# Kernel optimization log

Measured on AMD Instinct MI355X. Metric: run time of the kernel, lower is better.

## Reference

```python
import jax, jax.numpy as jnp
import numpy as np

HEADS = 8
B, N, DIM = 8, 1024, 128  # n must be a perfect square (H=W=32)
LN_EPS = 1e-5


def _region_means(xg):
    """Four-quadrant region means per position via integral image.
    xg: [b,H,W,d] -> [b,H,W,4,d]. For position (h,w) the torch code pools:
      r1 = x[:, :h+1, :w+1], r2 = x[:, :h+1, w:], r3 = x[:, h:, :w+1], r4 = x[:, h:, w:]
    """
    b, H, W, d = xg.shape
    # padded 2D prefix sum: P[:, i, j] = sum over rows<i, cols<j
    P = jnp.pad(jnp.cumsum(jnp.cumsum(xg, axis=1), axis=2),
                ((0, 0), (1, 0), (1, 0), (0, 0)))
    r1 = P[:, 1:, 1:]                                              # sum x[:h+1,:w+1]
    r2 = P[:, 1:, -1:] - P[:, 1:, :-1]                             # sum x[:h+1, w:]
    r3 = P[:, -1:, 1:] - P[:, :-1, 1:]                             # sum x[h:, :w+1]
    r4 = P[:, -1:, -1:] - P[:, :-1, -1:] - P[:, -1:, :-1] + P[:, :-1, :-1]
    ah = jnp.arange(H, dtype=xg.dtype)
    aw = jnp.arange(W, dtype=xg.dtype)
    hp1 = (ah + 1.0)[:, None]   # h+1
    wp1 = (aw + 1.0)[None, :]   # w+1
    hr = (H - ah)[:, None]      # H-h
    wr = (W - aw)[None, :]      # W-w
    c1 = (hp1 * wp1)[None, :, :, None]
    c2 = (hp1 * wr)[None, :, :, None]
    c3 = (hr * wp1)[None, :, :, None]
    c4 = (hr * wr)[None, :, :, None]
    return jnp.stack([r1 / c1, r2 / c2, r3 / c3, r4 / c4], axis=3)


def setup_inputs() -> dict:
    key = jax.random.key(0)
    ks = jax.random.split(key, 10)
    s = 0.02
    return {
        "x": jax.random.normal(ks[0], (B, N, DIM), jnp.float32),
        "ln_g": jnp.ones((DIM,), jnp.float32),
        "ln_b": jnp.zeros((DIM,), jnp.float32),
        "Wqkv": jax.random.normal(ks[1], (DIM, 3 * HEADS * DIM), jnp.float32) * s,
        "bqkv": jax.random.normal(ks[2], (3 * HEADS * DIM,), jnp.float32) * s,
        "Wq": jax.random.normal(ks[3], (DIM, DIM), jnp.float32) * s,
        "Wk": jax.random.normal(ks[4], (DIM, DIM), jnp.float32) * s,
        "Wv": jax.random.normal(ks[5], (DIM, DIM), jnp.float32) * s,
        "Wo": jax.random.normal(ks[6], (DIM, DIM), jnp.float32) * s,
        "bo": jax.random.normal(ks[7], (DIM,), jnp.float32) * s,
        "Wout": jax.random.normal(ks[8], (HEADS * DIM, DIM), jnp.float32) * s,
        "bout": jax.random.normal(ks[9], (DIM,), jnp.float32) * s,
    }


def reference(x, ln_g, ln_b, Wqkv, bqkv, Wq, Wk, Wv, Wo, bo, Wout, bout):
    b, n, dim = x.shape
    H = W = int(n ** 0.5)
    # LayerNorm
    mu = jnp.mean(x, axis=-1, keepdims=True)
    var = jnp.mean(jnp.square(x - mu), axis=-1, keepdims=True)
    xn = (x - mu) * jax.lax.rsqrt(var + LN_EPS) * ln_g + ln_b
    # qkv projection; only q is actually used downstream (k,v chunks are dead)
    qkv = xn @ Wqkv + bqkv
    q = qkv[..., : HEADS * dim].reshape(b, n, HEADS, dim).transpose(0, 2, 1, 3)  # [b,h,n,d]
    # region features, identical across heads -> keep unbroadcast [b,n,4,d]
    regions = _region_means(xn.reshape(b, H, W, dim)).reshape(b, n, 4, dim)
    # RegionAggregator
    qh = q @ Wq                                   # [b,h,n,d]
    k = jnp.einsum('bnrd,de->bnre', regions, Wk)  # [b,n,4,d]
    v = jnp.einsum('bnrd,de->bnre', regions, Wv)
    scale = (dim // HEADS) ** -0.5
    attn = jax.nn.softmax(jnp.einsum('bhnd,bnrd->bhnr', qh, k) * scale, axis=-1)
    agg = jnp.einsum('bhnr,bnrd->bhnd', attn, v)
    out = agg @ Wo + bo                           # [b,h,n,d]
    out = out.transpose(0, 2, 1, 3).reshape(b, n, HEADS * dim)
    return out @ Wout + bout
```

## Files before the change

kernel.cpp:

```cpp
#include <hip/hip_runtime.h>
#include <hip/hip_bf16.h>
#include <stdint.h>

#define HEADS 8
#define NN 1024
#define DIM 128
#define HW 32
#define LN_EPS 1e-5f

typedef __hip_bfloat16 bf16;
typedef __bf16 bf16x8 __attribute__((ext_vector_type(8)));
typedef float floatx4 __attribute__((ext_vector_type(4)));

__device__ __forceinline__ float b2f(bf16 v){ return __bfloat162float(v); }
__device__ __forceinline__ bf16 f2b(float v){ return __float2bfloat16(v); }

__device__ __forceinline__ float ldin(const void* p, size_t i, int f){
    return f ? ((const float*)p)[i] : b2f(((const bf16*)p)[i]);
}
__device__ __forceinline__ float4 ldin4(const void* p, size_t i, int f){
    if (f) return *reinterpret_cast<const float4*>((const float*)p + i);
    ushort4 u = *reinterpret_cast<const ushort4*>((const bf16*)p + i);
    float4 r;
    r.x = b2f(*(bf16*)&u.x); r.y = b2f(*(bf16*)&u.y);
    r.z = b2f(*(bf16*)&u.z); r.w = b2f(*(bf16*)&u.w);
    return r;
}
__device__ __forceinline__ int dtf(const void* g){
    return (((const uint32_t*)g)[0] == 0x3F800000u) ? 1 : 0;
}

__global__ __launch_bounds__(256) void ln_kernel(const void* __restrict__ x,
                                                 const void* __restrict__ g,
                                                 const void* __restrict__ bta,
                                                 bf16* __restrict__ xn){
    int f = dtf(g);
    int row = blockIdx.x*4 + (threadIdx.x >> 6);
    int lane = threadIdx.x & 63;
    size_t base = (size_t)row*DIM;
    float v0 = ldin(x, base+lane,    f);
    float v1 = ldin(x, base+lane+64, f);
    float s = v0+v1, ss = v0*v0+v1*v1;
    for (int o=32;o;o>>=1){ s += __shfl_xor(s,o,64); ss += __shfl_xor(ss,o,64); }
    float mu = s * (1.0f/DIM);
    float var = ss * (1.0f/DIM) - mu*mu;
    float rs = rsqrtf(var + LN_EPS);
    float y0 = (v0-mu)*rs*ldin(g,lane,f)    + ldin(bta,lane,f);
    float y1 = (v1-mu)*rs*ldin(g,lane+64,f) + ldin(bta,lane+64,f);
    xn[base+lane]    = f2b(y0);
    xn[base+lane+64] = f2b(y1);
}

__global__ __launch_bounds__(128) void rowscan_kernel(const bf16* __restrict__ xn,
                                                      float* __restrict__ P){
    int b = blockIdx.x >> 5, h = blockIdx.x & 31, c = threadIdx.x;
    const bf16* xr = xn + ((size_t)(b*NN + h*HW))*DIM + c;
    float* Pr = P + ((size_t)(b*NN + h*HW))*DIM + c;
    float run = 0.f;
    for (int w=0; w<HW; w++){ run += b2f(xr[(size_t)w*DIM]); Pr[(size_t)w*DIM] = run; }
}

__global__ __launch_bounds__(128) void colscan_kernel(float* __restrict__ P){
    int b = blockIdx.x >> 5, w = blockIdx.x & 31, c = threadIdx.x;
    float* Pc = P + ((size_t)(b*NN + w))*DIM + c;
    float run = 0.f;
    for (int h=0; h<HW; h++){
        size_t o = (size_t)h*HW*DIM;
        run += Pc[o]; Pc[o] = run;
    }
}

__global__ __launch_bounds__(256) void prep_kernel(const void* __restrict__ Wqkv,
                                                   const void* __restrict__ bqkv,
                                                   const void* __restrict__ Wq,
                                                   const void* __restrict__ Wk,
                                                   const void* __restrict__ Wv,
                                                   const void* __restrict__ Wo,
                                                   const void* __restrict__ bo,
                                                   const void* __restrict__ Wout,
                                                   const void* __restrict__ ln_g,
                                                   bf16* __restrict__ WhT,
                                                   bf16* __restrict__ WhoT,
                                                   bf16* __restrict__ WkvT,
                                                   float* __restrict__ bq,
                                                   float* __restrict__ bfin_part){
    __shared__ float S1[128][132];
    __shared__ float S2[8][132];
    int f = dtf(ln_g);
    int t = threadIdx.x;
    int blk = blockIdx.x;
    if (blk < 128){
        int h = blk >> 4, dc = blk & 15;
#pragma unroll
        for (int i=0;i<16;i++){
            int idx4 = (t + i*256)*4;
            int k = idx4 >> 7, e = idx4 & 127;
            *reinterpret_cast<float4*>(&S1[k][e]) = ldin4(Wq, idx4, f);
        }
        {
            int idx4 = t*4;
            int dl = idx4 >> 7, k = idx4 & 127;
            *reinterpret_cast<float4*>(&S2[dl][k]) =
                ldin4(Wqkv, (size_t)(dc*8+dl)*3072 + h*128 + k, f);
        }
        __syncthreads();
        int d = t & 7;
        int e0 = (t >> 3) * 4;
        float acc[4] = {0.f,0.f,0.f,0.f};
        for (int k=0;k<128;k++){
            float a = S2[d][k];
            float4 wv = *reinterpret_cast<const float4*>(&S1[k][e0]);
            acc[0] += a*wv.x; acc[1] += a*wv.y; acc[2] += a*wv.z; acc[3] += a*wv.w;
        }
#pragma unroll
        for (int i=0;i<4;i++)
            WhT[(size_t)(h*128 + e0 + i)*128 + dc*8 + d] = f2b(acc[i]);
    } else if (blk < 256){
        int h = (blk-128) >> 4, dc = (blk-128) & 15;
#pragma unroll
        for (int i=0;i<16;i++){
            int idx4 = (t + i*256)*4;
            int k = idx4 >> 7, e = idx4 & 127;
            *reinterpret_cast<float4*>(&S1[k][e]) =
                ldin4(Wout, (size_t)(h*128 + k)*128 + e, f);
        }
        {
            int idx4 = t*4;
            int dl = idx4 >> 7, k = idx4 & 127;
            *reinterpret_cast<float4*>(&S2[dl][k]) =
                ldin4(Wo, (size_t)(dc*8+dl)*128 + k, f);
        }
        __syncthreads();
        int d = t & 7;
        int e0 = (t >> 3) * 4;
        float acc[4] = {0.f,0.f,0.f,0.f};
        for (int k=0;k<128;k++){
            float a = S2[d][k];
            float4 wv = *reinterpret_cast<const float4*>(&S1[k][e0]);
            acc[0] += a*wv.x; acc[1] += a*wv.y; acc[2] += a*wv.z; acc[3] += a*wv.w;
        }
#pragma unroll
        for (int i=0;i<4;i++)
            WhoT[(size_t)(e0 + i)*1024 + h*128 + dc*8 + d] = f2b(acc[i]);
    } else {
        int sub = blk - 256;
        if (sub < 8){
            int h = sub;
            int e = t & 127, kh = t >> 7;
            float s = 0.f;
            for (int k=kh*64; k<kh*64+64; k++)
                s += ldin(bqkv, h*128 + k, f) * ldin(Wq, (size_t)k*128 + e, f);
            S1[kh][e] = s;
            __syncthreads();
            if (t < 128) bq[h*128 + t] = S1[0][t] + S1[1][t];
        } else if (sub < 16){
            int h = sub - 8;
            if (t < 128) S2[0][t] = ldin(bo, t, f);
            __syncthreads();
            int e = t & 127, half = t >> 7;
            float s = 0.f;
            for (int k = half*64; k < half*64 + 64; k++)
                s += S2[0][k] * ldin(Wout, (size_t)(h*128 + k)*128 + e, f);
            S1[half][e] = s;
            __syncthreads();
            if (t < 128) bfin_part[h*128 + t] = S1[0][t] + S1[1][t];
        } else {
            const void* W = (sub == 16) ? Wk : Wv;
            int base = (sub == 16) ? 0 : 128;
#pragma unroll
            for (int i=0;i<16;i++){
                int idx4 = (t + i*256)*4;
                int d = idx4 >> 7, e = idx4 & 127;
                *reinterpret_cast<float4*>(&S1[d][e]) = ldin4(W, idx4, f);
            }
            __syncthreads();
            for (int i=0;i<64;i++){
                int idx = t + i*256; int e = idx >> 7, d = idx & 127;
                WkvT[(size_t)(base + e)*128 + d] = f2b(S1[d][e]);
            }
        }
    }
}

__global__ __launch_bounds__(256) void gemm_mfma_kernel(const bf16* __restrict__ A,
                                                        const bf16* __restrict__ BT,
                                                        const float* __restrict__ bias,
                                                        bf16* __restrict__ C,
                                                        int M, int N, int K){
    __shared__ __align__(16) bf16 As[64][136];
    __shared__ __align__(16) bf16 Bs[64][136];
    int t = threadIdx.x;
    int w = t >> 6, lane = t & 63;
    int r = lane & 15, q = lane >> 4;
    int m0 = blockIdx.y * 64, n0 = blockIdx.x * 64;
    floatx4 acc[4];
#pragma unroll
    for (int nt=0;nt<4;nt++) acc[nt] = (floatx4){0.f,0.f,0.f,0.f};

    for (int kt = 0; kt < K; kt += 128){
#pragma unroll
        for (int c=0;c<4;c++){
            int id = t + c*256;
            int row = id >> 4, c8 = id & 15;
            *reinterpret_cast<uint4*>(&As[row][c8*8]) =
                *reinterpret_cast<const uint4*>(&A[(size_t)(m0+row)*K + kt + c8*8]);
            *reinterpret_cast<uint4*>(&Bs[row][c8*8]) =
                *reinterpret_cast<const uint4*>(&BT[(size_t)(n0+row)*K + kt + c8*8]);
        }
        __syncthreads();
#pragma unroll
        for (int kc=0;kc<4;kc++){
            bf16x8 a = *reinterpret_cast<const bf16x8*>(&As[w*16 + r][kc*32 + q*8]);
#pragma unroll
            for (int nt=0;nt<4;nt++){
                bf16x8 b = *reinterpret_cast<const bf16x8*>(&Bs[nt*16 + r][kc*32 + q*8]);
                acc[nt] = __builtin_amdgcn_mfma_f32_16x16x32_bf16(a, b, acc[nt], 0, 0, 0);
            }
        }
        __syncthreads();
    }
#pragma unroll
    for (int nt=0;nt<4;nt++){
#pragma unroll
        for (int i=0;i<4;i++){
            int row = m0 + w*16 + q*4 + i;
            int col = n0 + nt*16 + r;
            C[(size_t)row*N + col] = f2b(acc[nt][i] + (bias ? bias[col] : 0.f));
        }
    }
}

__global__ __launch_bounds__(256) void kvprobs_kernel(const float* __restrict__ P,
                                                      const bf16* __restrict__ WkvT,
                                                      const bf16* __restrict__ qh,
                                                      bf16* __restrict__ vmat,
                                                      float* __restrict__ probs){
    __shared__ __align__(16) char pool[52480];
    bf16 (*As)[136] = reinterpret_cast<bf16(*)[136]>(pool);
    bf16 (*Bs)[136] = reinterpret_cast<bf16(*)[136]>(pool + 17408);
    bf16 (*kS)[16][136] = reinterpret_cast<bf16(*)[16][136]>(pool);
    bf16 (*qhS)[1032]   = reinterpret_cast<bf16(*)[1032]>(pool + 17408);
    float* logits       = reinterpret_cast<float*>(pool + 50432);

    int t = threadIdx.x;
    int bn0 = blockIdx.x * 16;
    {
        int bn_local = t >> 4;
        int c0 = (t & 15) * 8;
        int bn = bn0 + bn_local;
        int b = bn >> 10, n = bn & 1023;
        int hh = n >> 5, ww = n & 31;
        const float* Pb = P + (size_t)b*NN*DIM;
        auto ld8 = [&](int h, int w, float* o){
            if (h==0 || w==0){
#pragma unroll
                for (int j=0;j<8;j++) o[j] = 0.f;
                return;
            }
            const float* p = Pb + ((size_t)((h-1)*HW + (w-1)))*DIM + c0;
            float4 u = *reinterpret_cast<const float4*>(p);
            float4 v = *reinterpret_cast<const float4*>(p+4);
            o[0]=u.x;o[1]=u.y;o[2]=u.z;o[3]=u.w;o[4]=v.x;o[5]=v.y;o[6]=v.z;o[7]=v.w;
        };
        float f_h1 = (float)(hh+1), f_w1 = (float)(ww+1);
        float f_hr = (float)(HW-hh), f_wr = (float)(HW-ww);
        float a0[8], a1[8];
        ld8(hh+1, ww+1, a0);
#pragma unroll
        for (int j=0;j<8;j++) As[bn_local*4 + 0][c0+j] = f2b(a0[j] / (f_h1*f_w1));
        ld8(hh+1, HW, a0); ld8(hh+1, ww, a1);
#pragma unroll
        for (int j=0;j<8;j++) As[bn_local*4 + 1][c0+j] = f2b((a0[j]-a1[j]) / (f_h1*f_wr));
        ld8(HW, ww+1, a0); ld8(hh, ww+1, a1);
#pragma unroll
        for (int j=0;j<8;j++) As[bn_local*4 + 2][c0+j] = f2b((a0[j]-a1[j]) / (f_hr*f_w1));
        float a2[8], a3[8];
        ld8(HW, HW, a0); ld8(hh, HW, a1); ld8(HW, ww, a2); ld8(hh, ww, a3);
#pragma unroll
        for (int j=0;j<8;j++)
            As[bn_local*4 + 3][c0+j] = f2b((a0[j]-a1[j]-a2[j]+a3[j]) / (f_hr*f_wr));
    }
    int w = t >> 6, lane = t & 63;
    int r = lane & 15, q = lane >> 4;
    floatx4 acc[16];
#pragma unroll
    for (int i=0;i<16;i++) acc[i] = (floatx4){0.f,0.f,0.f,0.f};
    for (int half=0; half<2; half++){
        __syncthreads();
#pragma unroll
        for (int i=0;i<8;i++){
            int id = t + i*256;
            int row = id >> 4, c8 = id & 15;
            *reinterpret_cast<uint4*>(&Bs[row][c8*8]) =
                *reinterpret_cast<const uint4*>(&WkvT[(size_t)(half*128 + row)*128 + c8*8]);
        }
        __syncthreads();
#pragma unroll
        for (int kc=0;kc<4;kc++){
            bf16x8 a = *reinterpret_cast<const bf16x8*>(&As[w*16 + r][kc*32 + q*8]);
#pragma unroll
            for (int nt=0;nt<8;nt++){
                bf16x8 b = *reinterpret_cast<const bf16x8*>(&Bs[nt*16 + r][kc*32 + q*8]);
                acc[half*8+nt] = __builtin_amdgcn_mfma_f32_16x16x32_bf16(a, b, acc[half*8+nt], 0, 0, 0);
            }
        }
    }
#pragma unroll
    for (int nt=0;nt<8;nt++){
#pragma unroll
        for (int i=0;i<4;i++){
            int row = bn0*4 + w*16 + q*4 + i;
            int col = nt*16 + r;
            vmat[(size_t)row*128 + col] = f2b(acc[8+nt][i]);
        }
    }
    __syncthreads();
#pragma unroll
    for (int nt=0;nt<8;nt++){
#pragma unroll
        for (int i=0;i<4;i++){
            int rowg = w*16 + q*4 + i;
            kS[rowg & 3][rowg >> 2][nt*16 + r] = f2b(acc[nt][i]);
        }
    }
#pragma unroll
    for (int i=0;i<8;i++){
        int id = t + i*256;
        int row = id >> 7, c8 = id & 127;
        *reinterpret_cast<uint4*>(&qhS[row][c8*8]) =
            *reinterpret_cast<const uint4*>(&qh[(size_t)(bn0+row)*1024 + c8*8]);
    }
    __syncthreads();
#pragma unroll
    for (int h2=0; h2<2; h2++){
        int h = w*2 + h2;
#pragma unroll
        for (int rg=0; rg<4; rg++){
            floatx4 s = (floatx4){0.f,0.f,0.f,0.f};
#pragma unroll
            for (int kc=0;kc<4;kc++){
                bf16x8 a = *reinterpret_cast<const bf16x8*>(&qhS[r][h*128 + kc*32 + q*8]);
                bf16x8 b = *reinterpret_cast<const bf16x8*>(&kS[rg][r][kc*32 + q*8]);
                s = __builtin_amdgcn_mfma_f32_16x16x32_bf16(a, b, s, 0, 0, 0);
            }
            if ((r >> 2) == q){
                int i = r & 3;
                float d = (i==0)?s[0]:(i==1)?s[1]:(i==2)?s[2]:s[3];
                logits[(r*8 + h)*4 + rg] = d;
            }
        }
    }
    __syncthreads();
    if (t < 128){
        int bn = t >> 3, h = t & 7;
        const float* L = &logits[(bn*8 + h)*4];
        float l0 = L[0]*0.25f, l1 = L[1]*0.25f, l2 = L[2]*0.25f, l3 = L[3]*0.25f;
        float m = fmaxf(fmaxf(l0,l1),fmaxf(l2,l3));
        float e0 = __expf(l0-m), e1=__expf(l1-m), e2=__expf(l2-m), e3=__expf(l3-m);
        float inv = 1.0f/(e0+e1+e2+e3);
        float4 pv = {e0*inv, e1*inv, e2*inv, e3*inv};
        *reinterpret_cast<float4*>(&probs[(size_t)(bn0+bn)*32 + h*4]) = pv;
    }
}

__global__ __launch_bounds__(256) void out_kernel(const float* __restrict__ probs,
                                                  const bf16* __restrict__ vmat,
                                                  const bf16* __restrict__ WhoT,
                                                  const float* __restrict__ bfin_part,
                                                  const void* __restrict__ bout,
                                                  const void* __restrict__ ln_g,
                                                  void* __restrict__ out){
    __shared__ __align__(16) bf16 v_lds[4][32][136];
    __shared__ __align__(16) bf16 Bs[128][136];
    __shared__ __align__(16) float p_lds[32][36];
    int f = dtf(ln_g);
    int t = threadIdx.x;
    int bn0 = blockIdx.x * 32;
#pragma unroll
    for (int i=0;i<8;i++){
        int id = t + i*256;
        int c8 = id & 15, row = (id >> 4) & 31, rg = id >> 9;
        *reinterpret_cast<uint4*>(&v_lds[rg][row][c8*8]) =
            *reinterpret_cast<const uint4*>(&vmat[(size_t)((bn0+row)*4 + rg)*128 + c8*8]);
    }
#pragma unroll
    for (int i=0;i<4;i++){
        int id = t + i*256;
        int row = id >> 5, col = id & 31;
        p_lds[row][col] = probs[(size_t)bn0*32 + id];
    }
    int w = t >> 6, lane = t & 63;
    int r = lane & 15, q = lane >> 4;
    int mh = w & 1, nh = w >> 1;
    int myrow = mh*16 + r;
    floatx4 acc[4];
#pragma unroll
    for (int nt=0;nt<4;nt++) acc[nt] = (floatx4){0.f,0.f,0.f,0.f};

    for (int h=0; h<8; h++){
        __syncthreads();
#pragma unroll
        for (int i=0;i<8;i++){
            int id = t + i*256;
            int row = id >> 4, c8 = id & 15;
            *reinterpret_cast<uint4*>(&Bs[row][c8*8]) =
                *reinterpret_cast<const uint4*>(&WhoT[(size_t)row*1024 + h*128 + c8*8]);
        }
        __syncthreads();
        float4 pv = *reinterpret_cast<const float4*>(&p_lds[myrow][h*4]);
#pragma unroll
        for (int kc=0;kc<4;kc++){
            int c = kc*32 + q*8;
            bf16x8 v0 = *reinterpret_cast<const bf16x8*>(&v_lds[0][myrow][c]);
            bf16x8 v1 = *reinterpret_cast<const bf16x8*>(&v_lds[1][myrow][c]);
            bf16x8 v2 = *reinterpret_cast<const bf16x8*>(&v_lds[2][myrow][c]);
            bf16x8 v3 = *reinterpret_cast<const bf16x8*>(&v_lds[3][myrow][c]);
            bf16x8 a;
#pragma unroll
            for (int j=0;j<8;j++){
                float s = pv.x*(float)v0[j] + pv.y*(float)v1[j]
                        + pv.z*(float)v2[j] + pv.w*(float)v3[j];
                a[j] = (__bf16)s;
            }
#pragma unroll
            for (int nt=0;nt<4;nt++){
                bf16x8 b = *reinterpret_cast<const bf16x8*>(&Bs[nh*64 + nt*16 + r][kc*32 + q*8]);
                acc[nt] = __builtin_amdgcn_mfma_f32_16x16x32_bf16(a, b, acc[nt], 0, 0, 0);
            }
        }
    }
#pragma unroll
    for (int nt=0;nt<4;nt++){
        int col = nh*64 + nt*16 + r;
        float bias = ldin(bout, col, f);
#pragma unroll
        for (int h=0;h<8;h++) bias += bfin_part[h*128 + col];
#pragma unroll
        for (int i=0;i<4;i++){
            int row = bn0 + mh*16 + q*4 + i;
            float v = acc[nt][i] + bias;
            if (f) ((float*)out)[(size_t)row*DIM + col] = v;
            else   ((bf16*)out)[(size_t)row*DIM + col] = f2b(v);
        }
    }
}

extern "C" void kernel_launch(void* const* d_in, const int* in_sizes, int n_in,
                              void* d_out, int out_size, void* d_ws, size_t ws_size,
                              hipStream_t stream){
    const void* x    = d_in[0];
    const void* ln_g = d_in[1];
    const void* ln_b = d_in[2];
    const void* Wqkv = d_in[3];
    const void* bqkv = d_in[4];
    const void* Wq   = d_in[5];
    const void* Wk   = d_in[6];
    const void* Wv   = d_in[7];
    const void* Wo   = d_in[8];
    const void* bo   = d_in[9];
    const void* Wout = d_in[10];
    const void* bout = d_in[11];

    char* ws = (char*)d_ws;
    size_t off = 0;
    auto alloc = [&](size_t bytes)->char*{
        char* p = ws + off; off += (bytes + 255) & ~size_t(255); return p;
    };
    bf16*  WhT   = (bf16*)alloc((size_t)1024*128*2);
    bf16*  WkvT  = (bf16*)alloc((size_t)256*128*2);
    bf16*  WhoT  = (bf16*)alloc((size_t)128*1024*2);
    float* bq    = (float*)alloc(1024*4);
    float* bfin_part = (float*)alloc(8*128*4);
    float* P     = (float*)alloc((size_t)8*NN*DIM*4);
    bf16*  xn    = (bf16*)alloc((size_t)8192*128*2);
    bf16*  qh    = (bf16*)alloc((size_t)8192*1024*2);
    bf16*  vmat  = (bf16*)alloc((size_t)32768*128*2);
    float* probs = (float*)alloc((size_t)8192*32*4);

    prep_kernel<<<274, 256, 0, stream>>>(Wqkv, bqkv, Wq, Wk, Wv, Wo, bo, Wout,
                                         ln_g, WhT, WhoT, WkvT, bq, bfin_part);
    ln_kernel<<<2048, 256, 0, stream>>>(x, ln_g, ln_b, xn);
    rowscan_kernel<<<256, 128, 0, stream>>>(xn, P);
    colscan_kernel<<<256, 128, 0, stream>>>(P);
    gemm_mfma_kernel<<<dim3(16, 128), 256, 0, stream>>>(xn, WhT, bq, qh, 8192, 1024, 128);
    kvprobs_kernel<<<512, 256, 0, stream>>>(P, WkvT, qh, vmat, probs);
    out_kernel<<<256, 256, 0, stream>>>(probs, vmat, WhoT, bfin_part, bout, ln_g, d_out);
}
```

Baseline: 151.0 us.

## Fold Wqkv·Wq·Wkᵀ into per-head matrices and drop the qh GEMM

```diff
diff --git a/kernel.cpp b/kernel.cpp
--- a/kernel.cpp
+++ b/kernel.cpp
@@ -79,29 +79,36 @@
                                                    const void* __restrict__ bo,
                                                    const void* __restrict__ Wout,
                                                    const void* __restrict__ ln_g,
-                                                   bf16* __restrict__ WhT,
                                                    bf16* __restrict__ WhoT,
-                                                   bf16* __restrict__ WkvT,
-                                                   float* __restrict__ bq,
+                                                   bf16* __restrict__ WvT,
+                                                   bf16* __restrict__ MT,
+                                                   float* __restrict__ ck,
                                                    float* __restrict__ bfin_part){
-    __shared__ float S1[128][132];
-    __shared__ float S2[8][132];
+    __shared__ __align__(16) char pool[71808];
+    float (*S1)[132] = reinterpret_cast<float(*)[132]>(pool);
+    float (*S2)[132] = reinterpret_cast<float(*)[132]>(pool + 67584);
+    bf16  (*T1)[136] = reinterpret_cast<bf16(*)[136]>(pool);
+    bf16  (*T2)[136] = reinterpret_cast<bf16(*)[136]>(pool + 34816);
     int f = dtf(ln_g);
     int t = threadIdx.x;
     int blk = blockIdx.x;
+    int w = t >> 6, lane = t & 63;
+    int r = lane & 15, q = lane >> 4;
+
     if (blk < 128){
         int h = blk >> 4, dc = blk & 15;
 #pragma unroll
         for (int i=0;i<16;i++){
             int idx4 = (t + i*256)*4;
             int k = idx4 >> 7, e = idx4 & 127;
-            *reinterpret_cast<float4*>(&S1[k][e]) = ldin4(Wq, idx4, f);
+            *reinterpret_cast<float4*>(&S1[k][e]) =
+                ldin4(Wout, (size_t)(h*128 + k)*128 + e, f);
         }
         {
             int idx4 = t*4;
             int dl = idx4 >> 7, k = idx4 & 127;
             *reinterpret_cast<float4*>(&S2[dl][k]) =
-                ldin4(Wqkv, (size_t)(dc*8+dl)*3072 + h*128 + k, f);
+                ldin4(Wo, (size_t)(dc*8+dl)*128 + k, f);
         }
         __syncthreads();
         int d = t & 7;
@@ -114,133 +121,123 @@
         }
 #pragma unroll
         for (int i=0;i<4;i++)
-            WhT[(size_t)(h*128 + e0 + i)*128 + dc*8 + d] = f2b(acc[i]);
-    } else if (blk < 256){
-        int h = (blk-128) >> 4, dc = (blk-128) & 15;
+            WhoT[(size_t)(e0 + i)*1024 + h*128 + dc*8 + d] = f2b(acc[i]);
+    } else if (blk < 136){
+        int h = blk - 128;
+        if (t < 128) S2[0][t] = ldin(bo, t, f);
+        __syncthreads();
+        int e = t & 127, half = t >> 7;
+        float s = 0.f;
+        for (int k = half*64; k < half*64 + 64; k++)
+            s += S2[0][k] * ldin(Wout, (size_t)(h*128 + k)*128 + e, f);
+        S1[half][e] = s;
+        __syncthreads();
+        if (t < 128) bfin_part[h*128 + t] = S1[0][t] + S1[1][t];
+    } else if (blk == 136){
 #pragma unroll
         for (int i=0;i<16;i++){
             int idx4 = (t + i*256)*4;
-            int k = idx4 >> 7, e = idx4 & 127;
-            *reinterpret_cast<float4*>(&S1[k][e]) =
-                ldin4(Wout, (size_t)(h*128 + k)*128 + e, f);
-        }
-        {
-            int idx4 = t*4;
-            int dl = idx4 >> 7, k = idx4 & 127;
-            *reinterpret_cast<float4*>(&S2[dl][k]) =
-                ldin4(Wo, (size_t)(dc*8+dl)*128 + k, f);
-        }
-        __syncthreads();
-        int d = t & 7;
-        int e0 = (t >> 3) * 4;
-        float acc[4] = {0.f,0.f,0.f,0.f};
-        for (int k=0;k<128;k++){
-            float a = S2[d][k];
-            float4 wv = *reinterpret_cast<const float4*>(&S1[k][e0]);
-            acc[0] += a*wv.x; acc[1] += a*wv.y; acc[2] += a*wv.z; acc[3] += a*wv.w;
-        }
+            int d = idx4 >> 7, e = idx4 & 127;
+            *reinterpret_cast<float4*>(&S1[d][e]) = ldin4(Wv, idx4, f);
+        }
+        __syncthreads();
+        for (int i=0;i<64;i++){
+            int idx = t + i*256; int e = idx >> 7, d = idx & 127;
+            WvT[(size_t)e*128 + d] = f2b(S1[d][e]);
+        }
+    } else {
+        int h = blk - 137;
+#pragma unroll
+        for (int i=0;i<16;i++){
+            int idx4 = (t + i*256)*4;
+            int row = idx4 >> 7, col = idx4 & 127;
+            float4 a = ldin4(Wq, idx4, f);
+            T1[row][col] = f2b(a.x); T1[row][col+1] = f2b(a.y);
+            T1[row][col+2] = f2b(a.z); T1[row][col+3] = f2b(a.w);
+            float4 b = ldin4(Wk, idx4, f);
+            T2[row][col] = f2b(b.x); T2[row][col+1] = f2b(b.y);
+            T2[row][col+2] = f2b(b.z); T2[row][col+3] = f2b(b.w);
+        }
+        __syncthreads();
+        floatx4 g[16];
+#pragma unroll
+        for (int i=0;i<16;i++) g[i] = (floatx4){0.f,0.f,0.f,0.f};
+#pragma unroll
+        for (int kc=0;kc<4;kc++){
+#pragma unroll
+            for (int mt=0;mt<2;mt++){
+                bf16x8 a = *reinterpret_cast<const bf16x8*>(&T1[w*32+mt*16+r][kc*32+q*8]);
+#pragma unroll
+                for (int nt=0;nt<8;nt++){
+                    bf16x8 b = *reinterpret_cast<const bf16x8*>(&T2[nt*16+r][kc*32+q*8]);
+                    g[mt*8+nt] = __builtin_amdgcn_mfma_f32_16x16x32_bf16(a, b, g[mt*8+nt], 0, 0, 0);
+                }
+            }
+        }
+        __syncthreads();
+#pragma unroll
+        for (int mt=0;mt<2;mt++)
+#pragma unroll
+        for (int nt=0;nt<8;nt++)
 #pragma unroll
         for (int i=0;i<4;i++)
-            WhoT[(size_t)(e0 + i)*1024 + h*128 + dc*8 + d] = f2b(acc[i]);
-    } else {
-        int sub = blk - 256;
-        if (sub < 8){
-            int h = sub;
-            int e = t & 127, kh = t >> 7;
+            T1[nt*16 + r][w*32 + mt*16 + q*4 + i] = f2b(g[mt*8+nt][i]);
+        __syncthreads();
+#pragma unroll
+        for (int i=0;i<16;i++){
+            int idx4 = (t + i*256)*4;
+            int d = idx4 >> 7, kk = idx4 & 127;
+            float4 a = ldin4(Wqkv, (size_t)d*3072 + h*128 + kk, f);
+            T2[d][kk] = f2b(a.x); T2[d][kk+1] = f2b(a.y);
+            T2[d][kk+2] = f2b(a.z); T2[d][kk+3] = f2b(a.w);
+        }
+        __syncthreads();
+        floatx4 m2[16];
+#pragma unroll
+        for (int i=0;i<16;i++) m2[i] = (floatx4){0.f,0.f,0.f,0.f};
+#pragma unroll
+        for (int kc=0;kc<4;kc++){
+#pragma unroll
+            for (int mt=0;mt<2;mt++){
+                bf16x8 a = *reinterpret_cast<const bf16x8*>(&T2[w*32+mt*16+r][kc*32+q*8]);
+#pragma unroll
+                for (int nt=0;nt<8;nt++){
+                    bf16x8 b = *reinterpret_cast<const bf16x8*>(&T1[nt*16+r][kc*32+q*8]);
+                    m2[mt*8+nt] = __builtin_amdgcn_mfma_f32_16x16x32_bf16(a, b, m2[mt*8+nt], 0, 0, 0);
+                }
+            }
+        }
+#pragma unroll
+        for (int mt=0;mt<2;mt++)
+#pragma unroll
+        for (int nt=0;nt<8;nt++)
+#pragma unroll
+        for (int i=0;i<4;i++){
+            int e = nt*16 + r, d = w*32 + mt*16 + q*4 + i;
+            MT[((size_t)h*128 + e)*128 + d] = f2b(m2[mt*8+nt][i]);
+        }
+        if (t < 128){
             float s = 0.f;
-            for (int k=kh*64; k<kh*64+64; k++)
-                s += ldin(bqkv, h*128 + k, f) * ldin(Wq, (size_t)k*128 + e, f);
-            S1[kh][e] = s;
-            __syncthreads();
-            if (t < 128) bq[h*128 + t] = S1[0][t] + S1[1][t];
-        } else if (sub < 16){
-            int h = sub - 8;
-            if (t < 128) S2[0][t] = ldin(bo, t, f);
-            __syncthreads();
-            int e = t & 127, half = t >> 7;
-            float s = 0.f;
-            for (int k = half*64; k < half*64 + 64; k++)
-                s += S2[0][k] * ldin(Wout, (size_t)(h*128 + k)*128 + e, f);
-            S1[half][e] = s;
-            __syncthreads();
-            if (t < 128) bfin_part[h*128 + t] = S1[0][t] + S1[1][t];
-        } else {
-            const void* W = (sub == 16) ? Wk : Wv;
-            int base = (sub == 16) ? 0 : 128;
-#pragma unroll
-            for (int i=0;i<16;i++){
-                int idx4 = (t + i*256)*4;
-                int d = idx4 >> 7, e = idx4 & 127;
-                *reinterpret_cast<float4*>(&S1[d][e]) = ldin4(W, idx4, f);
-            }
-            __syncthreads();
-            for (int i=0;i<64;i++){
-                int idx = t + i*256; int e = idx >> 7, d = idx & 127;
-                WkvT[(size_t)(base + e)*128 + d] = f2b(S1[d][e]);
-            }
-        }
-    }
-}
-
-__global__ __launch_bounds__(256) void gemm_mfma_kernel(const bf16* __restrict__ A,
-                                                        const bf16* __restrict__ BT,
-                                                        const float* __restrict__ bias,
-                                                        bf16* __restrict__ C,
-                                                        int M, int N, int K){
-    __shared__ __align__(16) bf16 As[64][136];
-    __shared__ __align__(16) bf16 Bs[64][136];
-    int t = threadIdx.x;
-    int w = t >> 6, lane = t & 63;
-    int r = lane & 15, q = lane >> 4;
-    int m0 = blockIdx.y * 64, n0 = blockIdx.x * 64;
-    floatx4 acc[4];
-#pragma unroll
-    for (int nt=0;nt<4;nt++) acc[nt] = (floatx4){0.f,0.f,0.f,0.f};
-
-    for (int kt = 0; kt < K; kt += 128){
-#pragma unroll
-        for (int c=0;c<4;c++){
-            int id = t + c*256;
-            int row = id >> 4, c8 = id & 15;
-            *reinterpret_cast<uint4*>(&As[row][c8*8]) =
-                *reinterpret_cast<const uint4*>(&A[(size_t)(m0+row)*K + kt + c8*8]);
-            *reinterpret_cast<uint4*>(&Bs[row][c8*8]) =
-                *reinterpret_cast<const uint4*>(&BT[(size_t)(n0+row)*K + kt + c8*8]);
-        }
-        __syncthreads();
-#pragma unroll
-        for (int kc=0;kc<4;kc++){
-            bf16x8 a = *reinterpret_cast<const bf16x8*>(&As[w*16 + r][kc*32 + q*8]);
-#pragma unroll
-            for (int nt=0;nt<4;nt++){
-                bf16x8 b = *reinterpret_cast<const bf16x8*>(&Bs[nt*16 + r][kc*32 + q*8]);
-                acc[nt] = __builtin_amdgcn_mfma_f32_16x16x32_bf16(a, b, acc[nt], 0, 0, 0);
-            }
-        }
-        __syncthreads();
-    }
-#pragma unroll
-    for (int nt=0;nt<4;nt++){
-#pragma unroll
-        for (int i=0;i<4;i++){
-            int row = m0 + w*16 + q*4 + i;
-            int col = n0 + nt*16 + r;
-            C[(size_t)row*N + col] = f2b(acc[nt][i] + (bias ? bias[col] : 0.f));
+            for (int kk=0;kk<128;kk++)
+                s += ldin(bqkv, h*128 + kk, f) * b2f(T1[t][kk]);
+            ck[h*128 + t] = s;
         }
     }
 }
 
 __global__ __launch_bounds__(256) void kvprobs_kernel(const float* __restrict__ P,
-                                                      const bf16* __restrict__ WkvT,
-                                                      const bf16* __restrict__ qh,
+                                                      const bf16* __restrict__ WvT,
+                                                      const bf16* __restrict__ xn,
+                                                      const bf16* __restrict__ MT,
+                                                      const float* __restrict__ ck,
                                                       bf16* __restrict__ vmat,
                                                       float* __restrict__ probs){
-    __shared__ __align__(16) char pool[52480];
-    bf16 (*As)[136] = reinterpret_cast<bf16(*)[136]>(pool);
-    bf16 (*Bs)[136] = reinterpret_cast<bf16(*)[136]>(pool + 17408);
-    bf16 (*kS)[16][136] = reinterpret_cast<bf16(*)[16][136]>(pool);
-    bf16 (*qhS)[1032]   = reinterpret_cast<bf16(*)[1032]>(pool + 17408);
-    float* logits       = reinterpret_cast<float*>(pool + 50432);
+    __shared__ __align__(16) char pool[59136];
+    bf16 (*As)[136]  = reinterpret_cast<bf16(*)[136]>(pool);
+    bf16 (*Bs)[136]  = reinterpret_cast<bf16(*)[136]>(pool + 17408);
+    bf16 (*xnS)[136] = reinterpret_cast<bf16(*)[136]>(pool + 52224);
+    float* ckS       = reinterpret_cast<float*>(pool + 56576);
+    float* lg        = reinterpret_cast<float*>(pool + 57088);
 
     int t = threadIdx.x;
     int bn0 = blockIdx.x * 16;
@@ -279,87 +276,96 @@
 #pragma unroll
         for (int j=0;j<8;j++)
             As[bn_local*4 + 3][c0+j] = f2b((a0[j]-a1[j]-a2[j]+a3[j]) / (f_hr*f_wr));
+        int row = t >> 4, c8 = t & 15;
+        *reinterpret_cast<uint4*>(&xnS[row][c8*8]) =
+            *reinterpret_cast<const uint4*>(&xn[(size_t)(bn0+row)*DIM + c8*8]);
     }
     int w = t >> 6, lane = t & 63;
     int r = lane & 15, q = lane >> 4;
-    floatx4 acc[16];
-#pragma unroll
-    for (int i=0;i<16;i++) acc[i] = (floatx4){0.f,0.f,0.f,0.f};
-    for (int half=0; half<2; half++){
+    floatx4 vacc[8];
+#pragma unroll
+    for (int i=0;i<8;i++) vacc[i] = (floatx4){0.f,0.f,0.f,0.f};
+    __syncthreads();
+#pragma unroll
+    for (int i=0;i<8;i++){
+        int id = t + i*256;
+        int row = id >> 4, c8 = id & 15;
+        *reinterpret_cast<uint4*>(&Bs[row][c8*8]) =
+            *reinterpret_cast<const uint4*>(&WvT[(size_t)row*128 + c8*8]);
+    }
+    __syncthreads();
+#pragma unroll
+    for (int kc=0;kc<4;kc++){
+        bf16x8 a = *reinterpret_cast<const bf16x8*>(&As[w*16 + r][kc*32 + q*8]);
+#pragma unroll
+        for (int nt=0;nt<8;nt++){
+            bf16x8 b = *reinterpret_cast<const bf16x8*>(&Bs[nt*16 + r][kc*32 + q*8]);
+            vacc[nt] = __builtin_amdgcn_mfma_f32_16x16x32_bf16(a, b, vacc[nt], 0, 0, 0);
+        }
+    }
+#pragma unroll
+    for (int nt=0;nt<8;nt++){
+#pragma unroll
+        for (int i=0;i<4;i++){
+            int row = bn0*4 + w*16 + q*4 + i;
+            int col = nt*16 + r;
+            vmat[(size_t)row*128 + col] = f2b(vacc[nt][i]);
+        }
+    }
+    for (int h=0; h<8; h++){
         __syncthreads();
 #pragma unroll
         for (int i=0;i<8;i++){
             int id = t + i*256;
             int row = id >> 4, c8 = id & 15;
             *reinterpret_cast<uint4*>(&Bs[row][c8*8]) =
-                *reinterpret_cast<const uint4*>(&WkvT[(size_t)(half*128 + row)*128 + c8*8]);
-        }
-        __syncthreads();
+                *reinterpret_cast<const uint4*>(&MT[((size_t)h*128 + row)*128 + c8*8]);
+        }
+        if (t < 128) ckS[t] = ck[h*128 + t];
+        __syncthreads();
+        floatx4 at[8];
+#pragma unroll
+        for (int i=0;i<8;i++) at[i] = (floatx4){0.f,0.f,0.f,0.f};
 #pragma unroll
         for (int kc=0;kc<4;kc++){
-            bf16x8 a = *reinterpret_cast<const bf16x8*>(&As[w*16 + r][kc*32 + q*8]);
+            bf16x8 a = *reinterpret_cast<const bf16x8*>(&xnS[r][kc*32 + q*8]);
 #pragma unroll
             for (int nt=0;nt<8;nt++){
                 bf16x8 b = *reinterpret_cast<const bf16x8*>(&Bs[nt*16 + r][kc*32 + q*8]);
-                acc[half*8+nt] = __builtin_amdgcn_mfma_f32_16x16x32_bf16(a, b, acc[half*8+nt], 0, 0, 0);
-            }
-        }
-    }
-#pragma unroll
-    for (int nt=0;nt<8;nt++){
-#pragma unroll
-        for (int i=0;i<4;i++){
-            int row = bn0*4 + w*16 + q*4 + i;
-            int col = nt*16 + r;
-            vmat[(size_t)row*128 + col] = f2b(acc[8+nt][i]);
-        }
-    }
-    __syncthreads();
-#pragma unroll
-    for (int nt=0;nt<8;nt++){
-#pragma unroll
-        for (int i=0;i<4;i++){
-            int rowg = w*16 + q*4 + i;
-            kS[rowg & 3][rowg >> 2][nt*16 + r] = f2b(acc[nt][i]);
-        }
-    }
-#pragma unroll
-    for (int i=0;i<8;i++){
-        int id = t + i*256;
-        int row = id >> 7, c8 = id & 127;
-        *reinterpret_cast<uint4*>(&qhS[row][c8*8]) =
-            *reinterpret_cast<const uint4*>(&qh[(size_t)(bn0+row)*1024 + c8*8]);
-    }
-    __syncthreads();
-#pragma unroll
-    for (int h2=0; h2<2; h2++){
-        int h = w*2 + h2;
-#pragma unroll
-        for (int rg=0; rg<4; rg++){
-            floatx4 s = (floatx4){0.f,0.f,0.f,0.f};
-#pragma unroll
-            for (int kc=0;kc<4;kc++){
-                bf16x8 a = *reinterpret_cast<const bf16x8*>(&qhS[r][h*128 + kc*32 + q*8]);
-                bf16x8 b = *reinterpret_cast<const bf16x8*>(&kS[rg][r][kc*32 + q*8]);
-                s = __builtin_amdgcn_mfma_f32_16x16x32_bf16(a, b, s, 0, 0, 0);
-            }
-            if ((r >> 2) == q){
-                int i = r & 3;
-                float d = (i==0)?s[0]:(i==1)?s[1]:(i==2)?s[2]:s[3];
-                logits[(r*8 + h)*4 + rg] = d;
-            }
+                at[nt] = __builtin_amdgcn_mfma_f32_16x16x32_bf16(a, b, at[nt], 0, 0, 0);
+            }
+        }
+        float p[4] = {0.f,0.f,0.f,0.f};
+#pragma unroll
+        for (int nt=0;nt<8;nt++){
+            int c = nt*16 + r;
+            float ckc = ckS[c];
+#pragma unroll
+            for (int i=0;i<4;i++){
+                float tv = at[nt][i] + ckc;
+                p[i] += tv * b2f(As[(q*4+i)*4 + w][c]);
+            }
+        }
+#pragma unroll
+        for (int o=1;o<16;o<<=1){
+#pragma unroll
+            for (int i=0;i<4;i++) p[i] += __shfl_xor(p[i], o, 64);
+        }
+        if (r == 0){
+#pragma unroll
+            for (int i=0;i<4;i++) lg[((q*4+i)*8 + h)*4 + w] = p[i];
         }
     }
     __syncthreads();
     if (t < 128){
-        int bn = t >> 3, h = t & 7;
-        const float* L = &logits[(bn*8 + h)*4];
+        int bn = t >> 3, hh = t & 7;
+        const float* L = &lg[(bn*8 + hh)*4];
         float l0 = L[0]*0.25f, l1 = L[1]*0.25f, l2 = L[2]*0.25f, l3 = L[3]*0.25f;
         float m = fmaxf(fmaxf(l0,l1),fmaxf(l2,l3));
         float e0 = __expf(l0-m), e1=__expf(l1-m), e2=__expf(l2-m), e3=__expf(l3-m);
         float inv = 1.0f/(e0+e1+e2+e3);
         float4 pv = {e0*inv, e1*inv, e2*inv, e3*inv};
-        *reinterpret_cast<float4*>(&probs[(size_t)(bn0+bn)*32 + h*4]) = pv;
+        *reinterpret_cast<float4*>(&probs[(size_t)(bn0+bn)*32 + hh*4]) = pv;
     }
 }
 
@@ -466,23 +472,21 @@
     auto alloc = [&](size_t bytes)->char*{
         char* p = ws + off; off += (bytes + 255) & ~size_t(255); return p;
     };
-    bf16*  WhT   = (bf16*)alloc((size_t)1024*128*2);
-    bf16*  WkvT  = (bf16*)alloc((size_t)256*128*2);
     bf16*  WhoT  = (bf16*)alloc((size_t)128*1024*2);
-    float* bq    = (float*)alloc(1024*4);
+    bf16*  WvT   = (bf16*)alloc((size_t)128*128*2);
+    bf16*  MT    = (bf16*)alloc((size_t)8*128*128*2);
+    float* ck    = (float*)alloc((size_t)8*128*4);
     float* bfin_part = (float*)alloc(8*128*4);
     float* P     = (float*)alloc((size_t)8*NN*DIM*4);
     bf16*  xn    = (bf16*)alloc((size_t)8192*128*2);
-    bf16*  qh    = (bf16*)alloc((size_t)8192*1024*2);
     bf16*  vmat  = (bf16*)alloc((size_t)32768*128*2);
     float* probs = (float*)alloc((size_t)8192*32*4);
 
-    prep_kernel<<<274, 256, 0, stream>>>(Wqkv, bqkv, Wq, Wk, Wv, Wo, bo, Wout,
-                                         ln_g, WhT, WhoT, WkvT, bq, bfin_part);
+    prep_kernel<<<145, 256, 0, stream>>>(Wqkv, bqkv, Wq, Wk, Wv, Wo, bo, Wout,
+                                         ln_g, WhoT, WvT, MT, ck, bfin_part);
     ln_kernel<<<2048, 256, 0, stream>>>(x, ln_g, ln_b, xn);
     rowscan_kernel<<<256, 128, 0, stream>>>(xn, P);
     colscan_kernel<<<256, 128, 0, stream>>>(P);
-    gemm_mfma_kernel<<<dim3(16, 128), 256, 0, stream>>>(xn, WhT, bq, qh, 8192, 1024, 128);
-    kvprobs_kernel<<<512, 256, 0, stream>>>(P, WkvT, qh, vmat, probs);
+    kvprobs_kernel<<<512, 256, 0, stream>>>(P, WvT, xn, MT, ck, vmat, probs);
     out_kernel<<<256, 256, 0, stream>>>(probs, vmat, WhoT, bfin_part, bout, ln_g, d_out);
 }
```

After: 178.5 us. +18.2%, slower.

## Fuse q projection into kvprobs kernel and merge layernorm with row scan

Applied to the files above, without the earlier changes.

```diff
diff --git a/kernel.cpp b/kernel.cpp
--- a/kernel.cpp
+++ b/kernel.cpp
@@ -30,34 +30,47 @@
     return (((const uint32_t*)g)[0] == 0x3F800000u) ? 1 : 0;
 }
 
-__global__ __launch_bounds__(256) void ln_kernel(const void* __restrict__ x,
-                                                 const void* __restrict__ g,
-                                                 const void* __restrict__ bta,
-                                                 bf16* __restrict__ xn){
+__global__ __launch_bounds__(256) void lnscan_kernel(const void* __restrict__ x,
+                                                     const void* __restrict__ g,
+                                                     const void* __restrict__ bta,
+                                                     bf16* __restrict__ xn,
+                                                     float* __restrict__ P){
+    __shared__ float lnv[32][128];
     int f = dtf(g);
-    int row = blockIdx.x*4 + (threadIdx.x >> 6);
-    int lane = threadIdx.x & 63;
-    size_t base = (size_t)row*DIM;
-    float v0 = ldin(x, base+lane,    f);
-    float v1 = ldin(x, base+lane+64, f);
-    float s = v0+v1, ss = v0*v0+v1*v1;
-    for (int o=32;o;o>>=1){ s += __shfl_xor(s,o,64); ss += __shfl_xor(ss,o,64); }
-    float mu = s * (1.0f/DIM);
-    float var = ss * (1.0f/DIM) - mu*mu;
-    float rs = rsqrtf(var + LN_EPS);
-    float y0 = (v0-mu)*rs*ldin(g,lane,f)    + ldin(bta,lane,f);
-    float y1 = (v1-mu)*rs*ldin(g,lane+64,f) + ldin(bta,lane+64,f);
-    xn[base+lane]    = f2b(y0);
-    xn[base+lane+64] = f2b(y1);
-}
-
-__global__ __launch_bounds__(128) void rowscan_kernel(const bf16* __restrict__ xn,
-                                                      float* __restrict__ P){
-    int b = blockIdx.x >> 5, h = blockIdx.x & 31, c = threadIdx.x;
-    const bf16* xr = xn + ((size_t)(b*NN + h*HW))*DIM + c;
-    float* Pr = P + ((size_t)(b*NN + h*HW))*DIM + c;
-    float run = 0.f;
-    for (int w=0; w<HW; w++){ run += b2f(xr[(size_t)w*DIM]); Pr[(size_t)w*DIM] = run; }
+    int b = blockIdx.x >> 5, hh = blockIdx.x & 31;
+    int wv = threadIdx.x >> 6, lane = threadIdx.x & 63;
+    float gl0 = ldin(g, lane, f),    gl1 = ldin(g, lane+64, f);
+    float bl0 = ldin(bta, lane, f),  bl1 = ldin(bta, lane+64, f);
+    size_t rowbase = (size_t)b*NN + (size_t)hh*HW;
+#pragma unroll
+    for (int rnd=0; rnd<8; rnd++){
+        int w = rnd*4 + wv;
+        size_t base = (rowbase + w)*DIM;
+        float v0 = ldin(x, base+lane,    f);
+        float v1 = ldin(x, base+lane+64, f);
+        float s = v0+v1, ss = v0*v0+v1*v1;
+        for (int o=32;o;o>>=1){ s += __shfl_xor(s,o,64); ss += __shfl_xor(ss,o,64); }
+        float mu = s * (1.0f/DIM);
+        float var = ss * (1.0f/DIM) - mu*mu;
+        float rs = rsqrtf(var + LN_EPS);
+        float y0 = (v0-mu)*rs*gl0 + bl0;
+        float y1 = (v1-mu)*rs*gl1 + bl1;
+        xn[base+lane]    = f2b(y0);
+        xn[base+lane+64] = f2b(y1);
+        lnv[w][lane]    = y0;
+        lnv[w][lane+64] = y1;
+    }
+    __syncthreads();
+    if (threadIdx.x < 128){
+        int c = threadIdx.x;
+        float run = 0.f;
+        float* Pr = P + rowbase*DIM + c;
+#pragma unroll
+        for (int w=0; w<HW; w++){
+            run += lnv[w][c];
+            Pr[(size_t)w*DIM] = run;
+        }
+    }
 }
 
 __global__ __launch_bounds__(128) void colscan_kernel(float* __restrict__ P){
@@ -182,65 +195,21 @@
     }
 }
 
-__global__ __launch_bounds__(256) void gemm_mfma_kernel(const bf16* __restrict__ A,
-                                                        const bf16* __restrict__ BT,
-                                                        const float* __restrict__ bias,
-                                                        bf16* __restrict__ C,
-                                                        int M, int N, int K){
-    __shared__ __align__(16) bf16 As[64][136];
-    __shared__ __align__(16) bf16 Bs[64][136];
-    int t = threadIdx.x;
-    int w = t >> 6, lane = t & 63;
-    int r = lane & 15, q = lane >> 4;
-    int m0 = blockIdx.y * 64, n0 = blockIdx.x * 64;
-    floatx4 acc[4];
-#pragma unroll
-    for (int nt=0;nt<4;nt++) acc[nt] = (floatx4){0.f,0.f,0.f,0.f};
-
-    for (int kt = 0; kt < K; kt += 128){
-#pragma unroll
-        for (int c=0;c<4;c++){
-            int id = t + c*256;
-            int row = id >> 4, c8 = id & 15;
-            *reinterpret_cast<uint4*>(&As[row][c8*8]) =
-                *reinterpret_cast<const uint4*>(&A[(size_t)(m0+row)*K + kt + c8*8]);
-            *reinterpret_cast<uint4*>(&Bs[row][c8*8]) =
-                *reinterpret_cast<const uint4*>(&BT[(size_t)(n0+row)*K + kt + c8*8]);
-        }
-        __syncthreads();
-#pragma unroll
-        for (int kc=0;kc<4;kc++){
-            bf16x8 a = *reinterpret_cast<const bf16x8*>(&As[w*16 + r][kc*32 + q*8]);
-#pragma unroll
-            for (int nt=0;nt<4;nt++){
-                bf16x8 b = *reinterpret_cast<const bf16x8*>(&Bs[nt*16 + r][kc*32 + q*8]);
-                acc[nt] = __builtin_amdgcn_mfma_f32_16x16x32_bf16(a, b, acc[nt], 0, 0, 0);
-            }
-        }
-        __syncthreads();
-    }
-#pragma unroll
-    for (int nt=0;nt<4;nt++){
-#pragma unroll
-        for (int i=0;i<4;i++){
-            int row = m0 + w*16 + q*4 + i;
-            int col = n0 + nt*16 + r;
-            C[(size_t)row*N + col] = f2b(acc[nt][i] + (bias ? bias[col] : 0.f));
-        }
-    }
-}
-
 __global__ __launch_bounds__(256) void kvprobs_kernel(const float* __restrict__ P,
                                                       const bf16* __restrict__ WkvT,
-                                                      const bf16* __restrict__ qh,
+                                                      const bf16* __restrict__ WhT,
+                                                      const float* __restrict__ bq,
+                                                      const bf16* __restrict__ xn,
                                                       bf16* __restrict__ vmat,
                                                       float* __restrict__ probs){
-    __shared__ __align__(16) char pool[52480];
-    bf16 (*As)[136] = reinterpret_cast<bf16(*)[136]>(pool);
-    bf16 (*Bs)[136] = reinterpret_cast<bf16(*)[136]>(pool + 17408);
+    __shared__ __align__(16) char pool[63488];
+    bf16 (*As)[136]     = reinterpret_cast<bf16(*)[136]>(pool);
     bf16 (*kS)[16][136] = reinterpret_cast<bf16(*)[16][136]>(pool);
-    bf16 (*qhS)[1032]   = reinterpret_cast<bf16(*)[1032]>(pool + 17408);
-    float* logits       = reinterpret_cast<float*>(pool + 50432);
+    bf16 (*Bs)[136]     = reinterpret_cast<bf16(*)[136]>(pool + 17408);
+    bf16 (*xnS)[136]    = reinterpret_cast<bf16(*)[136]>(pool + 52224);
+    bf16 (*qL)[136]     = reinterpret_cast<bf16(*)[136]>(pool + 56576);
+    float* bqS          = reinterpret_cast<float*>(pool + 60928);
+    float* logits       = reinterpret_cast<float*>(pool + 61440);
 
     int t = threadIdx.x;
     int bn0 = blockIdx.x * 16;
@@ -279,6 +248,8 @@
 #pragma unroll
         for (int j=0;j<8;j++)
             As[bn_local*4 + 3][c0+j] = f2b((a0[j]-a1[j]-a2[j]+a3[j]) / (f_hr*f_wr));
+        *reinterpret_cast<uint4*>(&xnS[t >> 4][(t & 15)*8]) =
+            *reinterpret_cast<const uint4*>(&xn[(size_t)(bn0 + (t >> 4))*DIM + (t & 15)*8]);
     }
     int w = t >> 6, lane = t & 63;
     int r = lane & 15, q = lane >> 4;
@@ -323,30 +294,50 @@
             kS[rowg & 3][rowg >> 2][nt*16 + r] = f2b(acc[nt][i]);
         }
     }
-#pragma unroll
-    for (int i=0;i<8;i++){
-        int id = t + i*256;
-        int row = id >> 7, c8 = id & 127;
-        *reinterpret_cast<uint4*>(&qhS[row][c8*8]) =
-            *reinterpret_cast<const uint4*>(&qh[(size_t)(bn0+row)*1024 + c8*8]);
-    }
-    __syncthreads();
-#pragma unroll
-    for (int h2=0; h2<2; h2++){
-        int h = w*2 + h2;
-#pragma unroll
-        for (int rg=0; rg<4; rg++){
+    for (int h=0; h<8; h++){
+#pragma unroll
+        for (int i=0;i<8;i++){
+            int id = t + i*256;
+            int row = id >> 4, c8 = id & 15;
+            *reinterpret_cast<uint4*>(&Bs[row][c8*8]) =
+                *reinterpret_cast<const uint4*>(&WhT[(size_t)(h*128 + row)*128 + c8*8]);
+        }
+        if (t < 128) bqS[t] = bq[h*128 + t];
+        __syncthreads();
+        floatx4 qa[2];
+        qa[0] = (floatx4){0.f,0.f,0.f,0.f};
+        qa[1] = (floatx4){0.f,0.f,0.f,0.f};
+#pragma unroll
+        for (int kc=0;kc<4;kc++){
+            bf16x8 a = *reinterpret_cast<const bf16x8*>(&xnS[r][kc*32 + q*8]);
+#pragma unroll
+            for (int nl=0;nl<2;nl++){
+                int nt = w*2 + nl;
+                bf16x8 b = *reinterpret_cast<const bf16x8*>(&Bs[nt*16 + r][kc*32 + q*8]);
+                qa[nl] = __builtin_amdgcn_mfma_f32_16x16x32_bf16(a, b, qa[nl], 0, 0, 0);
+            }
+        }
+#pragma unroll
+        for (int nl=0;nl<2;nl++){
+            int col = (w*2 + nl)*16 + r;
+            float bb = bqS[col];
+#pragma unroll
+            for (int i=0;i<4;i++)
+                qL[q*4 + i][col] = f2b(qa[nl][i] + bb);
+        }
+        __syncthreads();
+        {
             floatx4 s = (floatx4){0.f,0.f,0.f,0.f};
 #pragma unroll
             for (int kc=0;kc<4;kc++){
-                bf16x8 a = *reinterpret_cast<const bf16x8*>(&qhS[r][h*128 + kc*32 + q*8]);
-                bf16x8 b = *reinterpret_cast<const bf16x8*>(&kS[rg][r][kc*32 + q*8]);
+                bf16x8 a = *reinterpret_cast<const bf16x8*>(&qL[r][kc*32 + q*8]);
+                bf16x8 b = *reinterpret_cast<const bf16x8*>(&kS[w][r][kc*32 + q*8]);
                 s = __builtin_amdgcn_mfma_f32_16x16x32_bf16(a, b, s, 0, 0, 0);
             }
             if ((r >> 2) == q){
                 int i = r & 3;
                 float d = (i==0)?s[0]:(i==1)?s[1]:(i==2)?s[2]:s[3];
-                logits[(r*8 + h)*4 + rg] = d;
+                logits[(r*8 + h)*4 + w] = d;
             }
         }
     }
@@ -473,16 +464,13 @@
     float* bfin_part = (float*)alloc(8*128*4);
     float* P     = (float*)alloc((size_t)8*NN*DIM*4);
     bf16*  xn    = (bf16*)alloc((size_t)8192*128*2);
-    bf16*  qh    = (bf16*)alloc((size_t)8192*1024*2);
     bf16*  vmat  = (bf16*)alloc((size_t)32768*128*2);
     float* probs = (float*)alloc((size_t)8192*32*4);
 
     prep_kernel<<<274, 256, 0, stream>>>(Wqkv, bqkv, Wq, Wk, Wv, Wo, bo, Wout,
                                          ln_g, WhT, WhoT, WkvT, bq, bfin_part);
-    ln_kernel<<<2048, 256, 0, stream>>>(x, ln_g, ln_b, xn);
-    rowscan_kernel<<<256, 128, 0, stream>>>(xn, P);
+    lnscan_kernel<<<256, 256, 0, stream>>>(x, ln_g, ln_b, xn, P);
     colscan_kernel<<<256, 128, 0, stream>>>(P);
-    gemm_mfma_kernel<<<dim3(16, 128), 256, 0, stream>>>(xn, WhT, bq, qh, 8192, 1024, 128);
-    kvprobs_kernel<<<512, 256, 0, stream>>>(P, WkvT, qh, vmat, probs);
+    kvprobs_kernel<<<512, 256, 0, stream>>>(P, WkvT, WhT, bq, xn, vmat, probs);
     out_kernel<<<256, 256, 0, stream>>>(probs, vmat, WhoT, bfin_part, bout, ln_g, d_out);
 }
```

Result: no change. 153.5 us (+1.6%).
